# Performance work log

Measured on AMD Instinct MI355X. Metric: run time of the kernel, lower is better.

The kernel has to match this reference:

```python
import jax, jax.numpy as jnp
import numpy as np

B, S, HID = 1, 2048, 2048
H = 16
D_NOPE, D_ROPE, D_V = 128, 64, 128
Q_HEAD = D_NOPE + D_ROPE  # 192
QL, KVL = 1536, 512
EPS = 1e-6
SCALE = Q_HEAD ** -0.5


def rms_norm(x, w, eps=EPS):
    return x * jax.lax.rsqrt(jnp.mean(x * x, axis=-1, keepdims=True) + eps) * w


def rotate_half(x):
    h = x.shape[-1] // 2
    return jnp.concatenate([-x[..., h:], x[..., :h]], axis=-1)


def apply_rope(x, cos, sin):
    # DeepSeek de-interleave: view(..., d//2, 2).transpose(-1,-2).reshape == [even, odd]
    x = jnp.concatenate([x[..., 0::2], x[..., 1::2]], axis=-1)
    return x * cos + rotate_half(x) * sin


def setup_inputs() -> dict:
    key = jax.random.key(0)
    ks = jax.random.split(key, 8)
    x = jax.random.normal(ks[0], (B, S, HID), dtype=jnp.float32)
    # causal additive mask
    causal = jnp.tril(jnp.ones((S, S), dtype=bool))
    mask = jnp.where(causal, 0.0, -1e9).astype(jnp.float32)[None, None]
    position_ids = jnp.broadcast_to(jnp.arange(S, dtype=jnp.int32), (B, S))
    # RoPE caches, theta=10000
    inv_freq = 1.0 / (10000.0 ** (np.arange(0, D_ROPE, 2, dtype=np.float32) / D_ROPE))
    freqs = np.outer(np.arange(S, dtype=np.float32), inv_freq)
    emb = np.concatenate([freqs, freqs], axis=-1)
    cos = jnp.asarray(np.cos(emb), dtype=jnp.float32)
    sin = jnp.asarray(np.sin(emb), dtype=jnp.float32)
    w = lambda k, shp: (jax.random.normal(k, shp, dtype=jnp.float32) * 0.02)
    return {
        "x": x, "mask": mask, "position_ids": position_ids, "cos": cos, "sin": sin,
        "q_a_w": w(ks[1], (HID, QL)),
        "q_a_ln": jnp.ones((QL,), jnp.float32),
        "q_b_w": w(ks[2], (QL, H * Q_HEAD)),
        "kv_a_w": w(ks[3], (HID, KVL + D_ROPE)),
        "kv_a_ln": jnp.ones((KVL,), jnp.float32),
        "kv_b_w": w(ks[4], (KVL, H * (D_NOPE + D_V))),
        "o_w": w(ks[5], (H * D_V, HID)),
    }


def reference(x, mask, position_ids, cos, sin, q_a_w, q_a_ln, q_b_w, kv_a_w, kv_a_ln, kv_b_w, o_w):
    b, s, _ = x.shape
    # low-rank Q projection
    q = rms_norm(x @ q_a_w, q_a_ln) @ q_b_w            # [B,S,H*192]
    q = q.reshape(b, s, H, Q_HEAD).transpose(0, 2, 1, 3)  # [B,H,S,192]
    q_nope, q_pe = q[..., :D_NOPE], q[..., D_NOPE:]
    # compressed KV + decoupled rope key (MQA, shared across heads)
    ckv = x @ kv_a_w                                   # [B,S,512+64]
    c_norm = rms_norm(ckv[..., :KVL], kv_a_ln)         # [B,S,512]
    k_pe = ckv[..., KVL:][:, None]                     # [B,1,S,64]
    kv = (c_norm @ kv_b_w).reshape(b, s, H, D_NOPE + D_V).transpose(0, 2, 1, 3)
    k_nope, value = kv[..., :D_NOPE], kv[..., D_NOPE:]  # [B,H,S,128] each
    # rope
    cos_p = cos[position_ids][:, None]                 # [B,1,S,64]
    sin_p = sin[position_ids][:, None]
    q_pe = apply_rope(q_pe, cos_p, sin_p)
    k_pe = apply_rope(k_pe, cos_p, sin_p)
    query = jnp.concatenate([q_nope, q_pe], axis=-1)   # [B,H,S,192]
    key = jnp.concatenate([k_nope, jnp.broadcast_to(k_pe, (b, H, s, D_ROPE))], axis=-1)
    scores = jnp.einsum("bhsd,bhtd->bhst", query, key) * SCALE + mask
    attn = jax.nn.softmax(scores, axis=-1)
    out = jnp.einsum("bhst,bhtd->bhsd", attn, value)   # [B,H,S,128]
    out = out.transpose(0, 2, 1, 3).reshape(b, s, H * D_V) @ o_w
    kv_cache = jnp.concatenate([c_norm, k_pe[:, 0]], axis=-1)  # [B,S,576] latent cache
    return out, kv_cache
```

## Files before the change

kernel.cpp:

```cpp
#include <hip/hip_runtime.h>

typedef unsigned short u16;
typedef __bf16 bf16x8 __attribute__((ext_vector_type(8)));
typedef short s16x4 __attribute__((ext_vector_type(4)));
typedef short s16x8 __attribute__((ext_vector_type(8)));
typedef float f32x4 __attribute__((ext_vector_type(4)));

#define S_LEN 2048
#define NHEAD 16
#define QHEAD 192
#define EPS 1e-6f
#define ATTN_SCALE 0.07216878364870323f
#define QSCALE_LOG2E 0.10412011228586118f

__device__ __forceinline__ u16 f2bf(float f) {
    unsigned u = __builtin_bit_cast(unsigned, f);
    u = (u + 0x7FFFu + ((u >> 16) & 1u)) >> 16;
    return (u16)u;
}
__device__ __forceinline__ float bf2f(u16 h) {
    unsigned u = ((unsigned)h) << 16;
    return __builtin_bit_cast(float, u);
}

__device__ __forceinline__ void gl_lds16(const u16* g, u16* l) {
    __builtin_amdgcn_global_load_lds(
        (const __attribute__((address_space(1))) unsigned int*)g,
        (__attribute__((address_space(3))) unsigned int*)l,
        16, 0, 0);
}

#if defined(__has_builtin) && __has_builtin(__builtin_amdgcn_mfma_f32_16x16x16bf16_1k)
__device__ __forceinline__ f32x4 mfma16(s16x4 a, s16x4 b, f32x4 c) {
    return __builtin_amdgcn_mfma_f32_16x16x16bf16_1k(a, b, c, 0, 0, 0);
}
#else
__device__ __forceinline__ f32x4 mfma16(s16x4 a, s16x4 b, f32x4 c) {
    asm volatile("v_mfma_f32_16x16x16_bf16 %0, %1, %2, %0"
                 : "+v"(c) : "v"(a), "v"(b));
    return c;
}
#endif

template <int CF32>
__global__ __launch_bounds__(512, 4)
void gemm_bt(const u16* __restrict__ A, const u16* __restrict__ B,
             void* __restrict__ Cv, int K, int lda, int ldb, int ldc)
{
    const int tid = threadIdx.x;
    const int w = tid >> 6, lane = tid & 63;
    const int q = lane >> 4, r = lane & 15;
    const int tm = blockIdx.y, tn = blockIdx.x;

    __shared__ __align__(16) u16 smem[2 * 8192];

    const int lr = lane & 15;
    const int lc = (lane >> 4) * 8;
    const long ld = (w < 4) ? (long)lda : (long)ldb;
    const u16* g0 = ((w < 4)
        ? A + (long)(tm * 128 + w * 32 + lr) * lda
        : B + (long)(tn * 128 + (w - 4) * 32 + lr) * ldb) + lc;
    const u16* g1 = g0 + 16 * ld;
    const int s0 = w * 1024;
    const int s1 = s0 + 512;

    f32x4 acc[4][2] = {};
    const int wm = w >> 2;
    const int wn = w & 3;

    gl_lds16(g0, smem + s0);
    gl_lds16(g1, smem + s1);
    __syncthreads();

    int p = 0;
    for (int k0 = 0; k0 < K; k0 += 32) {
        u16* const cur = smem + p * 8192;
        u16* const nxt = smem + (p ^ 1) * 8192;
        if (k0 + 32 < K) {
            gl_lds16(g0 + k0 + 32, nxt + s0);
            gl_lds16(g1 + k0 + 32, nxt + s1);
        }
        bf16x8 af[4], bv[2];
        #pragma unroll
        for (int mt = 0; mt < 4; ++mt)
            af[mt] = *(const bf16x8*)&cur[(wm * 4 + mt) * 512 + lane * 8];
        #pragma unroll
        for (int nt = 0; nt < 2; ++nt)
            bv[nt] = *(const bf16x8*)&cur[4096 + (wn * 2 + nt) * 512 + lane * 8];
        #pragma unroll
        for (int mt = 0; mt < 4; ++mt)
            #pragma unroll
            for (int nt = 0; nt < 2; ++nt)
                acc[mt][nt] = __builtin_amdgcn_mfma_f32_16x16x32_bf16(
                    af[mt], bv[nt], acc[mt][nt], 0, 0, 0);
        __syncthreads();
        p ^= 1;
    }

    const int row0 = tm * 128 + wm * 64 + q * 4;
    const int col0 = tn * 128 + wn * 32 + r;
    if (CF32) {
        float* C = (float*)Cv;
        #pragma unroll
        for (int mt = 0; mt < 4; ++mt)
            #pragma unroll
            for (int i = 0; i < 4; ++i) {
                long rb = (long)(row0 + mt * 16 + i) * ldc + col0;
                #pragma unroll
                for (int nt = 0; nt < 2; ++nt)
                    C[rb + nt * 16] = acc[mt][nt][i];
            }
    } else {
        u16* C = (u16*)Cv;
        #pragma unroll
        for (int mt = 0; mt < 4; ++mt)
            #pragma unroll
            for (int i = 0; i < 4; ++i) {
                long rb = (long)(row0 + mt * 16 + i) * ldc + col0;
                #pragma unroll
                for (int nt = 0; nt < 2; ++nt)
                    C[rb + nt * 16] = f2bf(acc[mt][nt][i]);
            }
    }
}

template<int C0, int C1>
__device__ __forceinline__ void stage_tile(
    const u16* __restrict__ kvb, const u16* __restrict__ kpe,
    const u16* __restrict__ vt,
    u16* __restrict__ Kl, u16* __restrict__ Vl,
    int h, int t, int quad, int r)
{
    #pragma unroll
    for (int c = C0; c < C1; ++c) {
        if (c < 24) {
            const int mtk = c / 6, kc = c % 6;
            const int row = t * 64 + mtk * 16 + r;
            const u16* src = (kc < 4)
                ? kvb + (size_t)row * 4096 + h * 256 + kc * 32 + quad * 8
                : kpe + (size_t)row * 64 + (kc - 4) * 32 + quad * 8;
            gl_lds16(src, &Kl[c * 512]);
        } else {
            const int cv = c - 24, mtd = cv >> 1, sc = cv & 1;
            const u16* src = vt + ((size_t)h * 128 + mtd * 16 + r) * 2048
                             + t * 64 + sc * 32 + quad * 8;
            gl_lds16(src, &Vl[cv * 512]);
        }
    }
}

__device__ __forceinline__ void stage_dispatch(
    const u16* __restrict__ kvb, const u16* __restrict__ kpe,
    const u16* __restrict__ vt,
    u16* __restrict__ Kl, u16* __restrict__ Vl,
    int w, int h, int t, int quad, int r)
{
    if (w == 0)      stage_tile<0, 10>(kvb, kpe, vt, Kl, Vl, h, t, quad, r);
    else if (w == 1) stage_tile<10, 20>(kvb, kpe, vt, Kl, Vl, h, t, quad, r);
    else if (w == 2) stage_tile<20, 30>(kvb, kpe, vt, Kl, Vl, h, t, quad, r);
    else             stage_tile<30, 40>(kvb, kpe, vt, Kl, Vl, h, t, quad, r);
}

__device__ __forceinline__ void kv_tile_step(
    const u16* __restrict__ Kl, const u16* __restrict__ Vl,
    const bf16x8 (&Qf)[6], f32x4 (&Oacc)[8], float& lsum,
    int lane, int quad, int r, int kglob0, int qg, bool maskT)
{
    f32x4 Sacc[4];
    #pragma unroll
    for (int mtk = 0; mtk < 4; ++mtk)
        Sacc[mtk] = (f32x4){0.f, 0.f, 0.f, 0.f};
    #pragma unroll
    for (int kc = 0; kc < 6; ++kc)
        #pragma unroll
        for (int mtk = 0; mtk < 4; ++mtk) {
            bf16x8 Ak = *(const bf16x8*)&Kl[(mtk * 6 + kc) * 512 + lane * 8];
            Sacc[mtk] = __builtin_amdgcn_mfma_f32_16x16x32_bf16(
                Ak, Qf[kc], Sacc[mtk], 0, 0, 0);
        }
    #pragma unroll
    for (int sc = 0; sc < 2; ++sc) {
        s16x4 Pf[2];
        #pragma unroll
        for (int half = 0; half < 2; ++half) {
            const int kb = sc * 2 + half;
            const int kb0 = kglob0 + kb * 16 + quad * 4;
            #pragma unroll
            for (int i = 0; i < 4; ++i) {
                float pv = exp2f(Sacc[kb][i]);
                if (maskT && (kb0 + i > qg)) pv = 0.f;
                lsum += pv;
                Pf[half][i] = (short)f2bf(pv);
            }
        }
        #pragma unroll
        for (int mtd = 0; mtd < 8; ++mtd) {
            s16x8 Av8 = *(const s16x8*)&Vl[(mtd * 2 + sc) * 512 + quad * 128 + r * 8];
            s16x4 lo = __builtin_shufflevector(Av8, Av8, 0, 1, 2, 3);
            s16x4 hi = __builtin_shufflevector(Av8, Av8, 4, 5, 6, 7);
            Oacc[mtd] = mfma16(lo, Pf[0], Oacc[mtd]);
            Oacc[mtd] = mfma16(hi, Pf[1], Oacc[mtd]);
        }
    }
}

__global__ __launch_bounds__(256, 2)
void flash_attn(const u16* __restrict__ query, const u16* __restrict__ kvb,
                const u16* __restrict__ kpe, const u16* __restrict__ vt,
                u16* __restrict__ ao)
{
    const int tid = threadIdx.x;
    const int w = tid >> 6, lane = tid & 63;
    const int quad = lane >> 4, r = lane & 15;

    const int bid = (int)blockIdx.x;
    const int i = bid & 255;
    const int t_ = i >> 4;
    const int h = i & 15;
    const int j = (bid < 256) ? (31 - t_) : t_;

    const int q0 = j * 64;
    const int ntk = j + 1;

    __shared__ __align__(16) u16 smem[40960];

    const int qg = q0 + w * 16 + r;

    bf16x8 Qf[6];
    #pragma unroll
    for (int kc = 0; kc < 6; ++kc)
        Qf[kc] = *(const bf16x8*)(query
            + ((size_t)h * S_LEN + q0 + w * 16 + r) * QHEAD
            + kc * 32 + quad * 8);

    f32x4 Oacc[8];
    #pragma unroll
    for (int mtd = 0; mtd < 8; ++mtd)
        Oacc[mtd] = (f32x4){0.f, 0.f, 0.f, 0.f};
    float lsum = 0.f;

    stage_dispatch(kvb, kpe, vt, smem, smem + 12288, w, h, 0, quad, r);
    __syncthreads();

    for (int t = 0; t < ntk; ++t) {
        u16* const curb = smem + (t & 1) * 20480;
        u16* const nxtb = smem + ((t + 1) & 1) * 20480;
        if (t + 1 < ntk)
            stage_dispatch(kvb, kpe, vt, nxtb, nxtb + 12288, w, h, t + 1, quad, r);
        kv_tile_step(curb, curb + 12288, Qf, Oacc, lsum,
                     lane, quad, r, t * 64, qg, t == ntk - 1);
        __syncthreads();
    }

    float l = lsum;
    l += __shfl_xor(l, 16, 64);
    l += __shfl_xor(l, 32, 64);
    const float inv = 1.0f / l;
    const int qrow = q0 + w * 16 + r;
    #pragma unroll
    for (int mtd = 0; mtd < 8; ++mtd) {
        ushort4 o;
        o.x = f2bf(Oacc[mtd][0] * inv);
        o.y = f2bf(Oacc[mtd][1] * inv);
        o.z = f2bf(Oacc[mtd][2] * inv);
        o.w = f2bf(Oacc[mtd][3] * inv);
        *(ushort4*)(ao + (size_t)qrow * 2048 + h * 128 + mtd * 16 + quad * 4) = o;
    }
}

__global__ __launch_bounds__(256)
void cvt_f32_bf16(const float4* __restrict__ in, ushort4* __restrict__ out, int n4)
{
    int i = blockIdx.x * 256 + threadIdx.x;
    if (i < n4) {
        float4 v = in[i];
        ushort4 o;
        o.x = f2bf(v.x); o.y = f2bf(v.y); o.z = f2bf(v.z); o.w = f2bf(v.w);
        out[i] = o;
    }
}

__global__ __launch_bounds__(256)
void wtrans_k(const float* __restrict__ in, u16* __restrict__ out, int K, int N)
{
    __shared__ float tile[32][33];
    int k0 = blockIdx.x * 32, n0 = blockIdx.y * 32;
    int tx = threadIdx.x, ty = threadIdx.y;
    #pragma unroll
    for (int j = 0; j < 32; j += 8) {
        int n = n0 + tx;
        tile[ty + j][tx] = (n < N) ? in[(long)(k0 + ty + j) * N + n] : 0.0f;
    }
    __syncthreads();
    #pragma unroll
    for (int j = 0; j < 32; j += 8)
        out[(long)(n0 + ty + j) * K + k0 + tx] = f2bf(tile[tx][ty + j]);
}

__global__ __launch_bounds__(256)
void rmsnorm_k(u16* __restrict__ X, const float* __restrict__ w, int D, int ld)
{
    u16* row = X + (long)blockIdx.x * ld;
    const int tid = threadIdx.x;
    __shared__ float red[4];
    float sum = 0.f;
    for (int d = tid; d < D; d += 256) { float v = bf2f(row[d]); sum += v * v; }
    #pragma unroll
    for (int o = 32; o; o >>= 1) sum += __shfl_xor(sum, o, 64);
    if ((tid & 63) == 0) red[tid >> 6] = sum;
    __syncthreads();
    sum = red[0] + red[1] + red[2] + red[3];
    float scale = rsqrtf(sum / (float)D + EPS);
    for (int d = tid; d < D; d += 256)
        row[d] = f2bf(bf2f(row[d]) * scale * w[d]);
}

__global__ __launch_bounds__(256)
void kvcache_k(const u16* __restrict__ qkv, const float* __restrict__ ln,
               const int* __restrict__ pos_ids, const float* __restrict__ cosb,
               const float* __restrict__ sinb, float* __restrict__ kvout,
               u16* __restrict__ cnb, u16* __restrict__ kpe)
{
    const int s = blockIdx.x, tid = threadIdx.x;
    const u16* row = qkv + (long)s * 2176 + 1536;
    __shared__ float red[4];
    float sum = 0.f;
    for (int d = tid; d < 512; d += 256) { float v = bf2f(row[d]); sum += v * v; }
    #pragma unroll
    for (int o = 32; o; o >>= 1) sum += __shfl_xor(sum, o, 64);
    if ((tid & 63) == 0) red[tid >> 6] = sum;
    __syncthreads();
    sum = red[0] + red[1] + red[2] + red[3];
    float scale = rsqrtf(sum / 512.f + EPS);
    for (int d = tid; d < 512; d += 256) {
        float v = bf2f(row[d]) * scale * ln[d];
        kvout[(long)s * 576 + d] = v;
        cnb[(long)s * 512 + d] = f2bf(v);
    }
    if (tid < 32) {
        int p = pos_ids[s];
        float x0 = bf2f(row[512 + 2 * tid]);
        float x1 = bf2f(row[512 + 2 * tid + 1]);
        float c1 = cosb[p * 64 + tid], s1 = sinb[p * 64 + tid];
        float c2 = cosb[p * 64 + 32 + tid], s2 = sinb[p * 64 + 32 + tid];
        float lo = x0 * c1 - x1 * s1;
        float hi = x1 * c2 + x0 * s2;
        kvout[(long)s * 576 + 512 + tid] = lo;
        kvout[(long)s * 576 + 544 + tid] = hi;
        kpe[(long)s * 64 + tid] = f2bf(lo);
        kpe[(long)s * 64 + 32 + tid] = f2bf(hi);
    }
}

__global__ __launch_bounds__(256)
void qrope_k(const u16* __restrict__ qb, const int* __restrict__ pos_ids,
             const float* __restrict__ cosb, const float* __restrict__ sinb,
             u16* __restrict__ query)
{
    const int s = blockIdx.x, tid = threadIdx.x;
    const u16* row = qb + (long)s * 3072;
    {
        int h = tid >> 4, c = tid & 15;
        const u16* src = &row[h * QHEAD + c * 8];
        u16* dst = &query[((long)(h * S_LEN + s)) * QHEAD + c * 8];
        ushort4 a = *(const ushort4*)src;
        ushort4 b = *(const ushort4*)(src + 4);
        ushort4 oa, ob;
        oa.x = f2bf(bf2f(a.x) * QSCALE_LOG2E); oa.y = f2bf(bf2f(a.y) * QSCALE_LOG2E);
        oa.z = f2bf(bf2f(a.z) * QSCALE_LOG2E); oa.w = f2bf(bf2f(a.w) * QSCALE_LOG2E);
        ob.x = f2bf(bf2f(b.x) * QSCALE_LOG2E); ob.y = f2bf(bf2f(b.y) * QSCALE_LOG2E);
        ob.z = f2bf(bf2f(b.z) * QSCALE_LOG2E); ob.w = f2bf(bf2f(b.w) * QSCALE_LOG2E);
        *(ushort4*)dst = oa;
        *(ushort4*)(dst + 4) = ob;
    }
    int p = pos_ids[s];
    for (int idx = tid; idx < 512; idx += 256) {
        int h = idx >> 5, i = idx & 31;
        float x0 = bf2f(row[h * QHEAD + 128 + 2 * i]);
        float x1 = bf2f(row[h * QHEAD + 128 + 2 * i + 1]);
        float c1 = cosb[p * 64 + i], s1 = sinb[p * 64 + i];
        float c2 = cosb[p * 64 + 32 + i], s2 = sinb[p * 64 + 32 + i];
        u16* qr = query + ((long)(h * S_LEN + s)) * QHEAD;
        qr[128 + i] = f2bf((x0 * c1 - x1 * s1) * QSCALE_LOG2E);
        qr[160 + i] = f2bf((x1 * c2 + x0 * s2) * QSCALE_LOG2E);
    }
}

__global__ __launch_bounds__(256)
void vtrans_k(const u16* __restrict__ kv, u16* __restrict__ vt)
{
    __shared__ u16 tile[32][33];
    int s0 = blockIdx.x * 32, d0 = blockIdx.y * 32, h = blockIdx.z;
    int tx = threadIdx.x, ty = threadIdx.y;
    #pragma unroll
    for (int j = 0; j < 32; j += 8)
        tile[ty + j][tx] = kv[(long)(s0 + ty + j) * 4096 + h * 256 + 128 + d0 + tx];
    __syncthreads();
    const int txp = ((tx >> 2) & 3) * 8 + (tx >> 4) * 4 + (tx & 3);
    #pragma unroll
    for (int j = 0; j < 32; j += 8)
        vt[(long)(h * 128 + d0 + ty + j) * S_LEN + s0 + txp] = tile[tx][ty + j];
}

extern "C" void kernel_launch(void* const* d_in, const int* in_sizes, int n_in,
                              void* d_out, int out_size, void* d_ws, size_t ws_size,
                              hipStream_t stream)
{
    const float* x      = (const float*)d_in[0];
    const int*   posid  = (const int*)d_in[2];
    const float* cosb   = (const float*)d_in[3];
    const float* sinb   = (const float*)d_in[4];
    const float* q_a_w  = (const float*)d_in[5];
    const float* q_a_ln = (const float*)d_in[6];
    const float* q_b_w  = (const float*)d_in[7];
    const float* kv_a_w = (const float*)d_in[8];
    const float* kv_a_ln= (const float*)d_in[9];
    const float* kv_b_w = (const float*)d_in[10];
    const float* o_w    = (const float*)d_in[11];

    float* out    = (float*)d_out;
    float* kv_out = out + (size_t)2048 * 2048;

    char* ws = (char*)d_ws;
    size_t off = 0;
    auto alloc = [&](size_t bytes) { char* p = ws + off; off += (bytes + 255) & ~(size_t)255; return p; };
    u16* xb    = (u16*)alloc(2048ULL * 2048 * 2);
    u16* W1    = (u16*)alloc(2176ULL * 2048 * 2);
    u16* qbwt  = (u16*)alloc(3072ULL * 1536 * 2);
    u16* kvbwt = (u16*)alloc(4096ULL * 512 * 2);
    u16* owt   = (u16*)alloc(2048ULL * 2048 * 2);
    u16* qkv_a = (u16*)alloc(2048ULL * 2176 * 2);
    u16* qbuf  = (u16*)alloc(2048ULL * 3072 * 2);
    u16* query = (u16*)alloc(16ULL * 2048 * 192 * 2);
    u16* cnb   = (u16*)alloc(2048ULL * 512 * 2);
    u16* kpe   = (u16*)alloc(2048ULL * 64 * 2);
    u16* kvbuf = (u16*)alloc(2048ULL * 4096 * 2);
    u16* vt    = (u16*)alloc(16ULL * 128 * 2048 * 2);
    u16* ao    = (u16*)alloc(2048ULL * 2048 * 2);
    (void)ws_size; (void)in_sizes; (void)n_in; (void)out_size;

    dim3 blk(256);
    dim3 gblk(512);
    dim3 tblk(32, 8);

    cvt_f32_bf16<<<dim3(4096), blk, 0, stream>>>((const float4*)x, (ushort4*)xb, 2048 * 2048 / 4);
    wtrans_k<<<dim3(64, 48),  tblk, 0, stream>>>(q_a_w,  W1,                    2048, 1536);
    wtrans_k<<<dim3(64, 20),  tblk, 0, stream>>>(kv_a_w, W1 + 1536ULL * 2048,   2048, 576);
    wtrans_k<<<dim3(48, 96),  tblk, 0, stream>>>(q_b_w,  qbwt,  1536, 3072);
    wtrans_k<<<dim3(16, 128), tblk, 0, stream>>>(kv_b_w, kvbwt, 512,  4096);
    wtrans_k<<<dim3(64, 64),  tblk, 0, stream>>>(o_w,    owt,   2048, 2048);

    gemm_bt<0><<<dim3(17, 16), gblk, 0, stream>>>(xb, W1, qkv_a, 2048, 2048, 2048, 2176);
    rmsnorm_k<<<dim3(2048), blk, 0, stream>>>(qkv_a, q_a_ln, 1536, 2176);
    kvcache_k<<<dim3(2048), blk, 0, stream>>>(qkv_a, kv_a_ln, posid, cosb, sinb, kv_out, cnb, kpe);

    gemm_bt<0><<<dim3(24, 16), gblk, 0, stream>>>(qkv_a, qbwt, qbuf, 1536, 2176, 1536, 3072);
    qrope_k<<<dim3(2048), blk, 0, stream>>>(qbuf, posid, cosb, sinb, query);

    gemm_bt<0><<<dim3(32, 16), gblk, 0, stream>>>(cnb, kvbwt, kvbuf, 512, 512, 512, 4096);
    vtrans_k<<<dim3(64, 4, 16), tblk, 0, stream>>>(kvbuf, vt);

    flash_attn<<<dim3(512), dim3(256), 0, stream>>>(query, kvbuf, kpe, vt, ao);

    gemm_bt<1><<<dim3(16, 16), gblk, 0, stream>>>(ao, owt, out, 2048, 2048, 2048, 2048);
}
```

Before: 417.4 us.

## Triple-buffer GEMM LDS pipeline and merge q_b/kv_b GEMMs into one launch

The GEMM main loop moves from double buffering with a full __syncthreads per step to a three-stage LDS ring. Loads are issued two k-steps ahead, and each step waits with a partial vmcnt before a raw s_barrier, so global-to-LDS traffic overlaps more MFMA work. The q_b and kv_b projections, which are independent, now run in a single dual-GEMM launch split by blockIdx.z. This removes one launch and lets the two grids fill the GPU together. In exchange, LDS use grows from 32 KB to 48 KB per block, which may lower occupancy, and the dual launch includes idle early-exit blocks.

```diff
diff --git a/kernel.cpp b/kernel.cpp
--- a/kernel.cpp
+++ b/kernel.cpp
@@ -43,16 +43,14 @@
 #endif
 
 template <int CF32>
-__global__ __launch_bounds__(512, 4)
-void gemm_bt(const u16* __restrict__ A, const u16* __restrict__ B,
-             void* __restrict__ Cv, int K, int lda, int ldb, int ldc)
+__device__ __forceinline__ void gemm_core(
+    u16* __restrict__ smem,
+    const u16* __restrict__ A, const u16* __restrict__ B, void* __restrict__ Cv,
+    int K, int lda, int ldb, int ldc, int tm, int tn)
 {
     const int tid = threadIdx.x;
     const int w = tid >> 6, lane = tid & 63;
     const int q = lane >> 4, r = lane & 15;
-    const int tm = blockIdx.y, tn = blockIdx.x;
-
-    __shared__ __align__(16) u16 smem[2 * 8192];
 
     const int lr = lane & 15;
     const int lc = (lane >> 4) * 8;
@@ -67,18 +65,26 @@
     f32x4 acc[4][2] = {};
     const int wm = w >> 2;
     const int wn = w & 3;
+    const int n = K >> 5;
 
     gl_lds16(g0, smem + s0);
     gl_lds16(g1, smem + s1);
-    __syncthreads();
-
-    int p = 0;
-    for (int k0 = 0; k0 < K; k0 += 32) {
-        u16* const cur = smem + p * 8192;
-        u16* const nxt = smem + (p ^ 1) * 8192;
-        if (k0 + 32 < K) {
-            gl_lds16(g0 + k0 + 32, nxt + s0);
-            gl_lds16(g1 + k0 + 32, nxt + s1);
+    gl_lds16(g0 + 32, smem + 8192 + s0);
+    gl_lds16(g1 + 32, smem + 8192 + s1);
+    asm volatile("s_waitcnt vmcnt(2)" ::: "memory");
+    __builtin_amdgcn_sched_barrier(0);
+    __builtin_amdgcn_s_barrier();
+    __builtin_amdgcn_sched_barrier(0);
+
+    int bc = 0;
+    for (int t = 0; t < n; ++t) {
+        u16* const cur = smem + bc * 8192;
+        if (t + 2 < n) {
+            int bn = bc + 2; if (bn >= 3) bn -= 3;
+            u16* const nxt = smem + bn * 8192;
+            const long k2 = (long)(t + 2) << 5;
+            gl_lds16(g0 + k2, nxt + s0);
+            gl_lds16(g1 + k2, nxt + s1);
         }
         bf16x8 af[4], bv[2];
         #pragma unroll
@@ -93,8 +99,14 @@
             for (int nt = 0; nt < 2; ++nt)
                 acc[mt][nt] = __builtin_amdgcn_mfma_f32_16x16x32_bf16(
                     af[mt], bv[nt], acc[mt][nt], 0, 0, 0);
-        __syncthreads();
-        p ^= 1;
+        if (t + 1 < n) {
+            if (t + 2 < n) asm volatile("s_waitcnt vmcnt(2)" ::: "memory");
+            else           asm volatile("s_waitcnt vmcnt(0)" ::: "memory");
+            __builtin_amdgcn_sched_barrier(0);
+            __builtin_amdgcn_s_barrier();
+            __builtin_amdgcn_sched_barrier(0);
+        }
+        if (++bc == 3) bc = 0;
     }
 
     const int row0 = tm * 128 + wm * 64 + q * 4;
@@ -121,6 +133,31 @@
                 for (int nt = 0; nt < 2; ++nt)
                     C[rb + nt * 16] = f2bf(acc[mt][nt][i]);
             }
+    }
+}
+
+template <int CF32>
+__global__ __launch_bounds__(512, 4)
+void gemm_bt(const u16* __restrict__ A, const u16* __restrict__ B,
+             void* __restrict__ Cv, int K, int lda, int ldb, int ldc)
+{
+    __shared__ __align__(16) u16 smem[3 * 8192];
+    gemm_core<CF32>(smem, A, B, Cv, K, lda, ldb, ldc, blockIdx.y, blockIdx.x);
+}
+
+__global__ __launch_bounds__(512, 4)
+void gemm_bt_dual(const u16* __restrict__ A0, const u16* __restrict__ B0,
+                  void* __restrict__ C0, int K0, int lda0, int ldb0, int ldc0, int nx0,
+                  const u16* __restrict__ A1, const u16* __restrict__ B1,
+                  void* __restrict__ C1, int K1, int lda1, int ldb1, int ldc1, int nx1)
+{
+    __shared__ __align__(16) u16 smem[3 * 8192];
+    if (blockIdx.z == 0) {
+        if ((int)blockIdx.x >= nx0) return;
+        gemm_core<0>(smem, A0, B0, C0, K0, lda0, ldb0, ldc0, blockIdx.y, blockIdx.x);
+    } else {
+        if ((int)blockIdx.x >= nx1) return;
+        gemm_core<0>(smem, A1, B1, C1, K1, lda1, ldb1, ldc1, blockIdx.y, blockIdx.x);
     }
 }
 
@@ -454,10 +491,10 @@
     rmsnorm_k<<<dim3(2048), blk, 0, stream>>>(qkv_a, q_a_ln, 1536, 2176);
     kvcache_k<<<dim3(2048), blk, 0, stream>>>(qkv_a, kv_a_ln, posid, cosb, sinb, kv_out, cnb, kpe);
 
-    gemm_bt<0><<<dim3(24, 16), gblk, 0, stream>>>(qkv_a, qbwt, qbuf, 1536, 2176, 1536, 3072);
+    gemm_bt_dual<<<dim3(32, 16, 2), gblk, 0, stream>>>(
+        qkv_a, qbwt, qbuf, 1536, 2176, 1536, 3072, 24,
+        cnb, kvbwt, kvbuf, 512, 512, 512, 4096, 32);
     qrope_k<<<dim3(2048), blk, 0, stream>>>(qbuf, posid, cosb, sinb, query);
-
-    gemm_bt<0><<<dim3(32, 16), gblk, 0, stream>>>(cnb, kvbwt, kvbuf, 512, 512, 512, 4096);
     vtrans_k<<<dim3(64, 4, 16), tblk, 0, stream>>>(kvbuf, vt);
 
     flash_attn<<<dim3(512), dim3(256), 0, stream>>>(query, kvbuf, kpe, vt, ao);
```

Result: faster. 397.4 us (-4.8%).
